# Optimization experiments

Measured on AMD Instinct MI355X. Metric: run time of the kernel, lower is better.

Reference implementation:

```python
import jax, jax.numpy as jnp
import numpy as np

N_PUZZLES = 512
N = N_PUZZLES * 81          # nodes
E = N_PUZZLES * 81 * 20     # edges (20 peers per cell)
H = 96                      # mlp_hidden == lstm_hidden
DE = 16                     # edge feature / embed dim


def _lin(key, din, dout):
    kw, kb = jax.random.split(key)
    s = 1.0 / np.sqrt(din)
    W = jax.random.uniform(kw, (din, dout), jnp.float32, -s, s)
    b = jax.random.uniform(kb, (dout,), jnp.float32, -s, s)
    return W, b


def setup_inputs() -> dict:
    key = jax.random.key(0)
    ks = jax.random.split(key, 16)
    inp = {}
    inp["puzzle"] = jax.random.normal(ks[0], (N, DE), jnp.float32)
    inp["nodes"] = jax.random.normal(ks[1], (N, H), jnp.float32)
    inp["edge_features"] = jax.random.normal(ks[2], (E, DE), jnp.float32)
    inp["h"] = jax.random.normal(ks[3], (N, H), jnp.float32)
    inp["c"] = jax.random.normal(ks[4], (N, H), jnp.float32)
    inp["edges"] = jax.random.randint(ks[5], (E, 2), 0, N, jnp.int64)
    # message MLP: in = 2*H + DE
    inp["msg_W1"], inp["msg_b1"] = _lin(ks[6], 2 * H + DE, H)
    inp["msg_W2"], inp["msg_b2"] = _lin(ks[7], H, H)
    inp["msg_W3"], inp["msg_b3"] = _lin(ks[8], H, H)
    # post MLP: in = H + DE
    inp["post_W1"], inp["post_b1"] = _lin(ks[9], H + DE, H)
    inp["post_W2"], inp["post_b2"] = _lin(ks[10], H, H)
    inp["post_W3"], inp["post_b3"] = _lin(ks[11], H, H)
    # LSTM step (torch gate order i,f,g,o)
    inp["W_ih"], inp["b_ih"] = _lin(ks[12], H, 4 * H)
    inp["W_hh"], inp["b_hh"] = _lin(ks[13], H, 4 * H)
    # output linear 96 -> 10
    inp["out_W"], inp["out_b"] = _lin(ks[14], H, 10)
    return inp


def _mlp3(x, W1, b1, W2, b2, W3, b3):
    x = x @ W1 + b1
    x = jax.nn.relu(x) @ W2 + b2
    x = jax.nn.relu(x) @ W3 + b3
    return x


def reference(puzzle, nodes, edge_features, h, c, edges,
              msg_W1, msg_b1, msg_W2, msg_b2, msg_W3, msg_b3,
              post_W1, post_b1, post_W2, post_b2, post_W3, post_b3,
              W_ih, b_ih, W_hh, b_hh, out_W, out_b):
    src = edges[:, 0]
    dst = edges[:, 1]
    # gather -> MLP -> scatter-sum (message passing)
    msg_in = jnp.concatenate([nodes[src], nodes[dst], edge_features], axis=1)  # [E, 2H+DE]
    m = _mlp3(msg_in, msg_W1, msg_b1, msg_W2, msg_b2, msg_W3, msg_b3)          # [E, H]
    agg = jax.ops.segment_sum(m, src, num_segments=nodes.shape[0])             # [N, H]
    # post MLP on [messages, puzzle embedding]
    x = _mlp3(jnp.concatenate([agg, puzzle], axis=1),
              post_W1, post_b1, post_W2, post_b2, post_W3, post_b3)            # [N, H]
    # single LSTM step (torch gate order: i, f, g, o)
    gates = x @ W_ih + b_ih + h @ W_hh + b_hh                                  # [N, 4H]
    i, f, g, o = jnp.split(gates, 4, axis=1)
    c_new = jax.nn.sigmoid(f) * c + jax.nn.sigmoid(i) * jnp.tanh(g)
    h_new = jax.nn.sigmoid(o) * jnp.tanh(c_new)
    out = (h_new @ out_W + out_b).reshape(-1, 81, 10)                          # [B, 81, 10]
    return (h_new, h_new, c_new, out)
```

## Files before the change

### kernel.cpp

```cpp
#include <hip/hip_runtime.h>

#define NN 41472
#define NE 829440

typedef __attribute__((ext_vector_type(8))) short short8;
typedef __attribute__((ext_vector_type(4))) float f32x4;
typedef __attribute__((ext_vector_type(16))) float f32x16;
typedef __attribute__((ext_vector_type(4))) float float4v;
typedef __attribute__((ext_vector_type(4))) unsigned u32x4;

#define FLG_OFF   0
#define AGG_OFF   256
#define AGG_BYTES 15925248
#define W1F_OFF   (AGG_OFF + AGG_BYTES)
#define W2F_OFF   (W1F_OFF + 39936)
#define W3F_OFF   (W2F_OFF + 18432)
#define P1F_OFF   (W3F_OFF + 18432)
#define P2F_OFF   (P1F_OFF + 24576)
#define P3F_OFF   (P2F_OFF + 18432)
#define IHF_OFF   (P3F_OFF + 18432)
#define HHF_OFF   (IHF_OFF + 73728)
#define NB16_OFF  (HHF_OFF + 73728)
#define CUR_OFF   (NB16_OFF + 7962624)
#define BSUM_OFF  (CUR_OFF + 165888)
#define SRT_OFF   (BSUM_OFF + 256)
#define SID_OFF   (SRT_OFF + 6635520)
#define EFB_OFF   (SID_OFF + 3317760)
#define WS_NEED   (EFB_OFF + 26542080)

static __device__ __forceinline__ float bf2f(short s) {
  unsigned u = ((unsigned)(unsigned short)s) << 16;
  return __builtin_bit_cast(float, u);
}
static __device__ __forceinline__ short f2bf(float f) {
  unsigned u = __builtin_bit_cast(unsigned, f);
  unsigned r = (u + 0x7fffu + ((u >> 16) & 1u)) >> 16;
  return (short)r;
}
static __device__ __forceinline__ unsigned cvtpk(float lo, float hi) {
  unsigned r;
  asm("v_cvt_pk_bf16_f32 %0, %1, %2" : "=v"(r) : "v"(lo), "v"(hi));
  return r;
}
static __device__ __forceinline__ f32x4 fzero() { f32x4 z = {0.f, 0.f, 0.f, 0.f}; return z; }
static __device__ __forceinline__ f32x16 f16zero() {
  f32x16 z;
#pragma unroll
  for (int i = 0; i < 16; ++i) z[i] = 0.f;
  return z;
}
static __device__ __forceinline__ short8 szero() { short8 z = {0,0,0,0,0,0,0,0}; return z; }
static __device__ __forceinline__ float sigm(float x) { return 1.f / (1.f + __expf(-x)); }
static __device__ __forceinline__ float tanh_f(float x) {
  float ax = fabsf(x);
  float e  = __expf(-2.f * ax);
  float t  = (1.f - e) / (1.f + e);
  return copysignf(t, x);
}
static __device__ __forceinline__ int clampn(int v) {
  unsigned u = (unsigned)v;
  return (u < (unsigned)NN) ? v : 0;
}
static __device__ __forceinline__ float ldf(const void* base, size_t i, int f32) {
  return f32 ? ((const float*)base)[i] : bf2f(((const short*)base)[i]);
}
static __device__ __forceinline__ short8 ld8(const void* base, size_t i, int f32) {
  if (f32) {
    const float* p = (const float*)base + i;
    float4v a = *(const float4v*)p;
    float4v b = *(const float4v*)(p + 4);
    u32x4 u;
    u[0] = cvtpk(a[0], a[1]); u[1] = cvtpk(a[2], a[3]);
    u[2] = cvtpk(b[0], b[1]); u[3] = cvtpk(b[2], b[3]);
    return __builtin_bit_cast(short8, u);
  }
  return *(const short8*)((const short*)base + i);
}
static __device__ __forceinline__ short8 ldrow8(const void* base, size_t i, int f32) {
  if (f32) {
    const float* p = (const float*)base + i;
    short8 r;
#pragma unroll
    for (int j = 0; j < 8; ++j) r[j] = f2bf(p[j]);
    return r;
  }
  return *(const short8*)((const short*)base + i);
}
static __device__ __forceinline__ int ldedge(const int* e, int flat, int e64) {
  return e64 ? e[2 * flat] : e[flat];
}

__global__ __launch_bounds__(64) void sniff_kernel(const unsigned* __restrict__ nodes_u,
                                                   const int* __restrict__ edges_i,
                                                   int* __restrict__ flags) {
  int l = threadIdx.x;
  int votes = 0;
  for (int i = l; i < 256; i += 64) {
    unsigned u = nodes_u[i];
    int ex = (int)((u >> 23) & 0xFFu);
    if (ex >= 116 && ex <= 134) votes++;
  }
  int z = 0;
  for (int i = l; i < 128; i += 64) if (edges_i[2 * i + 1] == 0) z++;
#pragma unroll
  for (int o = 32; o; o >>= 1) { votes += __shfl_down(votes, o); z += __shfl_down(z, o); }
  if (l == 0) {
    flags[0] = (votes >= 160) ? 1 : 0;
    flags[1] = (z == 128) ? 1 : 0;
  }
}

__global__ __launch_bounds__(256) void zero_all_kernel(float4v* __restrict__ agg4,
                                                       int* __restrict__ cur) {
  int i = blockIdx.x * 256 + threadIdx.x;
  agg4[i] = float4v{0.f, 0.f, 0.f, 0.f};
  if (i < NN) cur[i] = 0;
}

__global__ __launch_bounds__(256) void nb16hist_kernel(const void* __restrict__ nodes,
                                                       const char* __restrict__ ws,
                                                       short8* __restrict__ out,
                                                       const int* __restrict__ edges,
                                                       int* __restrict__ cnt) {
  const int f32 = ((const int*)(ws + FLG_OFF))[0];
  const int e64 = ((const int*)(ws + FLG_OFF))[1];
  int gid = blockIdx.x * 256 + threadIdx.x;
  int s = clampn(ldedge(edges, 2 * gid, e64));
  atomicAdd(&cnt[s], 1);
  if (gid < NN * 96 / 8) out[gid] = ld8(nodes, (size_t)gid * 8, f32);
}

__global__ __launch_bounds__(1024) void scan_local_kernel(int* __restrict__ cnt,
                                                          int* __restrict__ bsum) {
  __shared__ int tmp[1024];
  const int t = threadIdx.x;
  const int i = blockIdx.x * 1024 + t;
  int v = (i < NN) ? cnt[i] : 0;
  tmp[t] = v;
  __syncthreads();
  for (int ofs = 1; ofs < 1024; ofs <<= 1) {
    int x = (t >= ofs) ? tmp[t - ofs] : 0;
    __syncthreads();
    tmp[t] += x;
    __syncthreads();
  }
  if (i < NN) cnt[i] = tmp[t] - v;
  if (t == 1023) bsum[blockIdx.x] = tmp[1023];
}

__global__ __launch_bounds__(64) void scan_tops_kernel(int* __restrict__ bsum, int nb) {
  int l = threadIdx.x;
  int v = (l < nb) ? bsum[l] : 0;
  int x = v;
#pragma unroll
  for (int o = 1; o < 64; o <<= 1) {
    int y = __shfl_up(x, o);
    if (l >= o) x += y;
  }
  if (l < nb) bsum[l] = x - v;
}

__global__ __launch_bounds__(1024) void scan_add_kernel(int* __restrict__ cnt,
                                                        const int* __restrict__ bsum) {
  int i = blockIdx.x * 1024 + threadIdx.x;
  if (i < NN) cnt[i] += bsum[blockIdx.x];
}

__global__ __launch_bounds__(256) void scatter_kernel(const int* __restrict__ edges,
                                                      const void* __restrict__ ef,
                                                      const char* __restrict__ ws,
                                                      int* __restrict__ cur,
                                                      int2* __restrict__ sdst,
                                                      short* __restrict__ efb) {
  const int f32 = ((const int*)(ws + FLG_OFF))[0];
  const int e64 = ((const int*)(ws + FLG_OFF))[1];
  int e = blockIdx.x * 256 + threadIdx.x;
  int s = clampn(ldedge(edges, 2 * e, e64));
  int d = clampn(ldedge(edges, 2 * e + 1, e64));
  int pos = atomicAdd(&cur[s], 1);
  sdst[pos] = make_int2(s, d);
  short8 lo = ld8(ef, (size_t)e * 16, f32);
  short8 hi = ld8(ef, (size_t)e * 16 + 8, f32);
  *(short8*)(efb + (size_t)pos * 16) = lo;
  *(short8*)(efb + (size_t)pos * 16 + 8) = hi;
}

__global__ __launch_bounds__(64) void relayout_kernel(
    const void* __restrict__ mW1, const void* __restrict__ mW2, const void* __restrict__ mW3,
    const void* __restrict__ pW1, const void* __restrict__ pW2, const void* __restrict__ pW3,
    const void* __restrict__ Wih, const void* __restrict__ Whh, char* __restrict__ ws)
{
  const int f32 = ((const int*)(ws + FLG_OFF))[0];
  int c = blockIdx.x;
  int l = threadIdx.x;
  const void* W; int K, NOUT, NT, fmt32; size_t off;
  if (c < 39)       {          W = mW1; K = 208; NOUT = 96;  NT = 3;  off = W1F_OFF; fmt32 = 1; }
  else if (c < 57)  { c -= 39;  W = mW2; K = 96;  NOUT = 96;  NT = 3;  off = W2F_OFF; fmt32 = 1; }
  else if (c < 75)  { c -= 57;  W = mW3; K = 96;  NOUT = 96;  NT = 3;  off = W3F_OFF; fmt32 = 1; }
  else if (c < 99)  { c -= 75;  W = pW1; K = 112; NOUT = 96;  NT = 6;  off = P1F_OFF; fmt32 = 0; }
  else if (c < 117) { c -= 99;  W = pW2; K = 96;  NOUT = 96;  NT = 6;  off = P2F_OFF; fmt32 = 0; }
  else if (c < 135) { c -= 117; W = pW3; K = 96;  NOUT = 96;  NT = 6;  off = P3F_OFF; fmt32 = 0; }
  else if (c < 207) { c -= 135; W = Wih; K = 96;  NOUT = 384; NT = 24; off = IHF_OFF; fmt32 = 0; }
  else              { c -= 207; W = Whh; K = 96;  NOUT = 384; NT = 24; off = HHF_OFF; fmt32 = 0; }
  int ks = c / NT, nt = c % NT;
  short8 v;
#pragma unroll
  for (int j = 0; j < 8; ++j) {
    int k, n;
    if (fmt32) { k = ks * 16 + (l >> 5) * 8 + j; n = nt * 32 + (l & 31); }
    else       { k = ks * 32 + (l >> 4) * 8 + j; n = nt * 16 + (l & 15); }
    v[j] = (k < K) ? f2bf(ldf(W, (size_t)k * NOUT + n, f32)) : (short)0;
  }
  short8* dst = (short8*)(ws + off);
  dst[c * 64 + l] = v;
}

template<int SORTED>
__global__ __launch_bounds__(256, 2) void edge_kernel(
    const void* __restrict__ nodes, const void* __restrict__ ef,
    const int* __restrict__ edges,
    const void* __restrict__ b1, const void* __restrict__ b2, const void* __restrict__ b3,
    const char* __restrict__ ws, float* __restrict__ agg)
{
  __shared__ __align__(16) short w2f[9216];
  __shared__ __align__(16) short w3f[9216];
  __shared__ __align__(16) short act[4][3328];

  const int f32 = ((const int*)(ws + FLG_OFF))[0];
  const int e64 = ((const int*)(ws + FLG_OFF))[1];
  const short* nb16 = (const short*)(ws + NB16_OFF);
  const int2*  sdst = (const int2*)(ws + SRT_OFF);
  const short* efb  = (const short*)(ws + EFB_OFF);

  {
    const short8* s2 = (const short8*)(ws + W2F_OFF);
    const short8* s3 = (const short8*)(ws + W3F_OFF);
    short8* d2 = (short8*)w2f;
    short8* d3 = (short8*)w3f;
    for (int i = threadIdx.x; i < 1152; i += 256) d2[i] = s2[i];
    for (int i = threadIdx.x; i < 1152; i += 256) d3[i] = s3[i];
  }
  __syncthreads();

  const int wv  = threadIdx.x >> 6;
  const int l   = threadIdx.x & 63;
  const int e31 = l & 31;
  const int hi  = l >> 5;
  short* aw = act[wv];
  const short8* w1g = (const short8*)(ws + W1F_OFF);

  const float B1[3] = {ldf(b1, e31, f32), ldf(b1, 32 + e31, f32), ldf(b1, 64 + e31, f32)};
  const float B2[3] = {ldf(b2, e31, f32), ldf(b2, 32 + e31, f32), ldf(b2, 64 + e31, f32)};
  const float B3[3] = {ldf(b3, e31, f32), ldf(b3, 32 + e31, f32), ldf(b3, 64 + e31, f32)};

  const int nbat = NE / 128;
  const int chunk = (nbat + gridDim.x - 1) / gridDim.x;
  const int it0 = blockIdx.x * chunk;
  int it1 = it0 + chunk; if (it1 > nbat) it1 = nbat;

  for (int it = it0; it < it1; ++it) {
    const int base = it * 128 + wv * 32;
    const int eL = base + e31;
    int src, dst;
    if (SORTED) {
      int2 sd = sdst[eL];
      src = clampn(sd.x); dst = clampn(sd.y);
    } else {
      src = clampn(ldedge(edges, 2 * eL, e64));
      dst = clampn(ldedge(edges, 2 * eL + 1, e64));
    }

    f32x16 a0 = f16zero(), a1 = f16zero(), a2 = f16zero();

#pragma unroll
    for (int ks = 0; ks < 6; ++ks) {
      short8 a = SORTED ? *(const short8*)(nb16 + (size_t)src * 96 + ks * 16 + hi * 8)
                        : ld8(nodes, (size_t)src * 96 + ks * 16 + hi * 8, f32);
      a0 = __builtin_amdgcn_mfma_f32_32x32x16_bf16(a, w1g[(ks * 3 + 0) * 64 + l], a0, 0, 0, 0);
      a1 = __builtin_amdgcn_mfma_f32_32x32x16_bf16(a, w1g[(ks * 3 + 1) * 64 + l], a1, 0, 0, 0);
      a2 = __builtin_amdgcn_mfma_f32_32x32x16_bf16(a, w1g[(ks * 3 + 2) * 64 + l], a2, 0, 0, 0);
    }
#pragma unroll
    for (int ks = 6; ks < 12; ++ks) {
      short8 a = SORTED ? *(const short8*)(nb16 + (size_t)dst * 96 + (ks - 6) * 16 + hi * 8)
                        : ld8(nodes, (size_t)dst * 96 + (ks - 6) * 16 + hi * 8, f32);
      a0 = __builtin_amdgcn_mfma_f32_32x32x16_bf16(a, w1g[(ks * 3 + 0) * 64 + l], a0, 0, 0, 0);
      a1 = __builtin_amdgcn_mfma_f32_32x32x16_bf16(a, w1g[(ks * 3 + 1) * 64 + l], a1, 0, 0, 0);
      a2 = __builtin_amdgcn_mfma_f32_32x32x16_bf16(a, w1g[(ks * 3 + 2) * 64 + l], a2, 0, 0, 0);
    }
    {
      short8 a = SORTED ? *(const short8*)(efb + (size_t)eL * 16 + hi * 8)
                        : ld8(ef, (size_t)eL * 16 + hi * 8, f32);
      a0 = __builtin_amdgcn_mfma_f32_32x32x16_bf16(a, w1g[(12 * 3 + 0) * 64 + l], a0, 0, 0, 0);
      a1 = __builtin_amdgcn_mfma_f32_32x32x16_bf16(a, w1g[(12 * 3 + 1) * 64 + l], a1, 0, 0, 0);
      a2 = __builtin_amdgcn_mfma_f32_32x32x16_bf16(a, w1g[(12 * 3 + 2) * 64 + l], a2, 0, 0, 0);
    }
#pragma unroll
    for (int r = 0; r < 16; ++r) {
      int row = (r & 3) + 8 * (r >> 2) + 4 * hi;
      aw[row * 104 +  0 + e31] = f2bf(fmaxf(a0[r] + B1[0], 0.f));
      aw[row * 104 + 32 + e31] = f2bf(fmaxf(a1[r] + B1[1], 0.f));
      aw[row * 104 + 64 + e31] = f2bf(fmaxf(a2[r] + B1[2], 0.f));
    }
    asm volatile("s_waitcnt lgkmcnt(0)" ::: "memory");
    __builtin_amdgcn_sched_barrier(0);

    f32x16 c0 = f16zero(), c1 = f16zero(), c2 = f16zero();
#pragma unroll
    for (int ks = 0; ks < 6; ++ks) {
      short8 a = *(const short8*)&aw[e31 * 104 + ks * 16 + hi * 8];
      c0 = __builtin_amdgcn_mfma_f32_32x32x16_bf16(a, *(const short8*)&w2f[((ks * 3 + 0) * 64 + l) * 8], c0, 0, 0, 0);
      c1 = __builtin_amdgcn_mfma_f32_32x32x16_bf16(a, *(const short8*)&w2f[((ks * 3 + 1) * 64 + l) * 8], c1, 0, 0, 0);
      c2 = __builtin_amdgcn_mfma_f32_32x32x16_bf16(a, *(const short8*)&w2f[((ks * 3 + 2) * 64 + l) * 8], c2, 0, 0, 0);
    }
#pragma unroll
    for (int r = 0; r < 16; ++r) {
      int row = (r & 3) + 8 * (r >> 2) + 4 * hi;
      aw[row * 104 +  0 + e31] = f2bf(fmaxf(c0[r] + B2[0], 0.f));
      aw[row * 104 + 32 + e31] = f2bf(fmaxf(c1[r] + B2[1], 0.f));
      aw[row * 104 + 64 + e31] = f2bf(fmaxf(c2[r] + B2[2], 0.f));
    }
    asm volatile("s_waitcnt lgkmcnt(0)" ::: "memory");
    __builtin_amdgcn_sched_barrier(0);

    f32x16 d0 = f16zero(), d1 = f16zero(), d2 = f16zero();
#pragma unroll
    for (int ks = 0; ks < 6; ++ks) {
      short8 a = *(const short8*)&aw[e31 * 104 + ks * 16 + hi * 8];
      d0 = __builtin_amdgcn_mfma_f32_32x32x16_bf16(a, *(const short8*)&w3f[((ks * 3 + 0) * 64 + l) * 8], d0, 0, 0, 0);
      d1 = __builtin_amdgcn_mfma_f32_32x32x16_bf16(a, *(const short8*)&w3f[((ks * 3 + 1) * 64 + l) * 8], d1, 0, 0, 0);
      d2 = __builtin_amdgcn_mfma_f32_32x32x16_bf16(a, *(const short8*)&w3f[((ks * 3 + 2) * 64 + l) * 8], d2, 0, 0, 0);
    }
    asm volatile("s_waitcnt lgkmcnt(0)" ::: "memory");
    __builtin_amdgcn_sched_barrier(0);

    if (SORTED) {
      float s0 = 0.f, s1 = 0.f, s2 = 0.f;
      int cu = -1, cnt = 0;
#pragma unroll
      for (int g = 0; g < 8; ++g) {
#pragma unroll
        for (int j = 0; j < 4; ++j) {
          const int reg = (g >> 1) * 4 + j;
          float t0 = d0[reg], t1 = d1[reg], t2 = d2[reg];
          float p0 = __shfl(t0, l ^ 32, 64);
          float p1 = __shfl(t1, l ^ 32, 64);
          float p2 = __shfl(t2, l ^ 32, 64);
          float v0 = ((g & 1) == hi) ? t0 : p0;
          float v1 = ((g & 1) == hi) ? t1 : p1;
          float v2 = ((g & 1) == hi) ? t2 : p2;
          int nd = __shfl(src, 4 * g + j, 64);
          if (nd == cu) {
            s0 += v0; s1 += v1; s2 += v2; cnt++;
          } else {
            if (hi == 0 && cu >= 0) {
              atomicAdd(&agg[(size_t)cu * 96 +      e31], s0 + cnt * B3[0]);
              atomicAdd(&agg[(size_t)cu * 96 + 32 + e31], s1 + cnt * B3[1]);
              atomicAdd(&agg[(size_t)cu * 96 + 64 + e31], s2 + cnt * B3[2]);
            }
            cu = nd; s0 = v0; s1 = v1; s2 = v2; cnt = 1;
          }
        }
      }
      if (hi == 0 && cu >= 0) {
        atomicAdd(&agg[(size_t)cu * 96 +      e31], s0 + cnt * B3[0]);
        atomicAdd(&agg[(size_t)cu * 96 + 32 + e31], s1 + cnt * B3[1]);
        atomicAdd(&agg[(size_t)cu * 96 + 64 + e31], s2 + cnt * B3[2]);
      }
    } else {
#pragma unroll
      for (int r = 0; r < 16; ++r) {
        int row = (r & 3) + 8 * (r >> 2) + 4 * hi;
        int s = clampn(ldedge(edges, 2 * (base + row), e64));
        atomicAdd(&agg[(size_t)s * 96 +      e31], d0[r] + B3[0]);
        atomicAdd(&agg[(size_t)s * 96 + 32 + e31], d1[r] + B3[1]);
        atomicAdd(&agg[(size_t)s * 96 + 64 + e31], d2[r] + B3[2]);
      }
    }
  }
}

__global__ __launch_bounds__(512, 1) void node_kernel(
    const float* __restrict__ agg, const void* __restrict__ puzzle,
    const void* __restrict__ h, const void* __restrict__ c,
    const void* __restrict__ pb1, const void* __restrict__ pb2, const void* __restrict__ pb3,
    const void* __restrict__ bih, const void* __restrict__ bhh,
    const void* __restrict__ oW, const void* __restrict__ ob,
    const char* __restrict__ ws,
    float* __restrict__ oh0, float* __restrict__ oh1, float* __restrict__ oc,
    float* __restrict__ oo)
{
  __shared__ __align__(16) short p2f[9216];
  __shared__ __align__(16) short p3f[9216];
  __shared__ __align__(16) short act[8][16][104];

  const int f32 = ((const int*)(ws + FLG_OFF))[0];

  {
    const short8* s2 = (const short8*)(ws + P2F_OFF);
    const short8* s3 = (const short8*)(ws + P3F_OFF);
    short8* d2 = (short8*)p2f;
    short8* d3 = (short8*)p3f;
    for (int i = threadIdx.x; i < 1152; i += 512) d2[i] = s2[i];
    for (int i = threadIdx.x; i < 1152; i += 512) d3[i] = s3[i];
  }
  __syncthreads();

  const int wv = threadIdx.x >> 6;
  const int l  = threadIdx.x & 63;
  const int lg = l >> 4, lr = l & 15;
  const int n0 = blockIdx.x * 128 + wv * 16;
  const int row = n0 + lr;

  const short8* p1g = (const short8*)(ws + P1F_OFF);
  const short8* ihg = (const short8*)(ws + IHF_OFF);
  const short8* hhg = (const short8*)(ws + HHF_OFF);

  f32x4 acc[6];
#pragma unroll
  for (int nt = 0; nt < 6; ++nt) acc[nt] = fzero();

#pragma unroll
  for (int ks = 0; ks < 3; ++ks) {
    const float* p = agg + (size_t)row * 96 + ks * 32 + lg * 8;
    short8 ahi, alo;
#pragma unroll
    for (int j = 0; j < 8; ++j) {
      float v = p[j];
      short hiq = f2bf(v);
      ahi[j] = hiq;
      alo[j] = f2bf(v - bf2f(hiq));
    }
#pragma unroll
    for (int nt = 0; nt < 6; ++nt) {
      short8 b = p1g[(ks * 6 + nt) * 64 + l];
      acc[nt] = __builtin_amdgcn_mfma_f32_16x16x32_bf16(ahi, b, acc[nt], 0, 0, 0);
      acc[nt] = __builtin_amdgcn_mfma_f32_16x16x32_bf16(alo, b, acc[nt], 0, 0, 0);
    }
  }
  {
    short8 a;
    if (lg < 2) a = ldrow8(puzzle, (size_t)row * 16 + lg * 8, f32);
    else        a = szero();
#pragma unroll
    for (int nt = 0; nt < 6; ++nt) {
      short8 b = p1g[(3 * 6 + nt) * 64 + l];
      acc[nt] = __builtin_amdgcn_mfma_f32_16x16x32_bf16(a, b, acc[nt], 0, 0, 0);
    }
  }
#pragma unroll
  for (int nt = 0; nt < 6; ++nt) {
    float bb = ldf(pb1, nt * 16 + lr, f32);
#pragma unroll
    for (int r = 0; r < 4; ++r) {
      float v = fmaxf(acc[nt][r] + bb, 0.f);
      act[wv][lg * 4 + r][nt * 16 + lr] = f2bf(v);
    }
    acc[nt] = fzero();
  }
  __syncthreads();

#pragma unroll
  for (int ks = 0; ks < 3; ++ks) {
    short8 a = *(const short8*)&act[wv][lr][ks * 32 + lg * 8];
#pragma unroll
    for (int nt = 0; nt < 6; ++nt) {
      short8 b = *(const short8*)&p2f[((ks * 6 + nt) * 64 + l) * 8];
      acc[nt] = __builtin_amdgcn_mfma_f32_16x16x32_bf16(a, b, acc[nt], 0, 0, 0);
    }
  }
  __syncthreads();
#pragma unroll
  for (int nt = 0; nt < 6; ++nt) {
    float bb = ldf(pb2, nt * 16 + lr, f32);
#pragma unroll
    for (int r = 0; r < 4; ++r) {
      float v = fmaxf(acc[nt][r] + bb, 0.f);
      act[wv][lg * 4 + r][nt * 16 + lr] = f2bf(v);
    }
    acc[nt] = fzero();
  }
  __syncthreads();

#pragma unroll
  for (int ks = 0; ks < 3; ++ks) {
    short8 a = *(const short8*)&act[wv][lr][ks * 32 + lg * 8];
#pragma unroll
    for (int nt = 0; nt < 6; ++nt) {
      short8 b = *(const short8*)&p3f[((ks * 6 + nt) * 64 + l) * 8];
      acc[nt] = __builtin_amdgcn_mfma_f32_16x16x32_bf16(a, b, acc[nt], 0, 0, 0);
    }
  }
  __syncthreads();
#pragma unroll
  for (int nt = 0; nt < 6; ++nt) {
    float bb = ldf(pb3, nt * 16 + lr, f32);
#pragma unroll
    for (int r = 0; r < 4; ++r) {
      act[wv][lg * 4 + r][nt * 16 + lr] = f2bf(acc[nt][r] + bb);
    }
  }
  __syncthreads();

  f32x4 g[24];
#pragma unroll
  for (int nt = 0; nt < 24; ++nt) g[nt] = fzero();
#pragma unroll
  for (int ks = 0; ks < 3; ++ks) {
    short8 ax = *(const short8*)&act[wv][lr][ks * 32 + lg * 8];
    short8 ah = ldrow8(h, (size_t)row * 96 + ks * 32 + lg * 8, f32);
#pragma unroll
    for (int nt = 0; nt < 24; ++nt) {
      short8 bi = ihg[(ks * 24 + nt) * 64 + l];
      g[nt] = __builtin_amdgcn_mfma_f32_16x16x32_bf16(ax, bi, g[nt], 0, 0, 0);
      short8 bh = hhg[(ks * 24 + nt) * 64 + l];
      g[nt] = __builtin_amdgcn_mfma_f32_16x16x32_bf16(ah, bh, g[nt], 0, 0, 0);
    }
  }

#pragma unroll
  for (int nt = 0; nt < 6; ++nt) {
    int col = nt * 16 + lr;
    float bi_i = ldf(bih, col, f32)       + ldf(bhh, col, f32);
    float bi_f = ldf(bih, 96 + col, f32)  + ldf(bhh, 96 + col, f32);
    float bi_g = ldf(bih, 192 + col, f32) + ldf(bhh, 192 + col, f32);
    float bi_o = ldf(bih, 288 + col, f32) + ldf(bhh, 288 + col, f32);
#pragma unroll
    for (int r = 0; r < 4; ++r) {
      int node = n0 + lg * 4 + r;
      float iv = g[nt][r]      + bi_i;
      float fv = g[nt + 6][r]  + bi_f;
      float gv = g[nt + 12][r] + bi_g;
      float ov = g[nt + 18][r] + bi_o;
      float cv = ldf(c, (size_t)node * 96 + col, f32);
      float cn = sigm(fv) * cv + sigm(iv) * tanh_f(gv);
      float hn = sigm(ov) * tanh_f(cn);
      oh0[(size_t)node * 96 + col] = hn;
      oh1[(size_t)node * 96 + col] = hn;
      oc [(size_t)node * 96 + col] = cn;
      act[wv][lg * 4 + r][col] = f2bf(hn);
    }
  }
  __syncthreads();

  const int nb0 = blockIdx.x * 128;
  for (int idx = threadIdx.x; idx < 1280; idx += 512) {
    int node16 = idx / 10;
    int o = idx - node16 * 10;
    const short* hrow = &act[node16 >> 4][node16 & 15][0];
    float a2 = ldf(ob, o, f32);
    for (int k = 0; k < 96; ++k)
      a2 = fmaf(bf2f(hrow[k]), ldf(oW, (size_t)k * 10 + o, f32), a2);
    oo[(size_t)(nb0 + node16) * 10 + o] = a2;
  }
}

extern "C" void kernel_launch(void* const* d_in, const int* in_sizes, int n_in,
                              void* d_out, int out_size, void* d_ws, size_t ws_size,
                              hipStream_t stream)
{
  const void* puzzle = d_in[0];
  const void* nodes  = d_in[1];
  const void* ef     = d_in[2];
  const void* h      = d_in[3];
  const void* c      = d_in[4];
  const int*  edges  = (const int*)d_in[5];
  const void* mW1 = d_in[6];  const void* mb1 = d_in[7];
  const void* mW2 = d_in[8];  const void* mb2 = d_in[9];
  const void* mW3 = d_in[10]; const void* mb3 = d_in[11];
  const void* pW1 = d_in[12]; const void* pb1 = d_in[13];
  const void* pW2 = d_in[14]; const void* pb2 = d_in[15];
  const void* pW3 = d_in[16]; const void* pb3 = d_in[17];
  const void* Wih = d_in[18]; const void* bih = d_in[19];
  const void* Whh = d_in[20]; const void* bhh = d_in[21];
  const void* oW  = d_in[22]; const void* ob  = d_in[23];

  char*  ws  = (char*)d_ws;
  int* flags = (int*)(ws + FLG_OFF);
  float* agg = (float*)(ws + AGG_OFF);
  int* cur = (int*)(ws + CUR_OFF);
  float* out = (float*)d_out;
  float* oh0 = out;
  float* oh1 = out + (size_t)NN * 96;
  float* oc  = out + (size_t)2 * NN * 96;
  float* oo  = out + (size_t)3 * NN * 96;

  sniff_kernel<<<1, 64, 0, stream>>>((const unsigned*)nodes, edges, flags);
  zero_all_kernel<<<3888, 256, 0, stream>>>((float4v*)agg, cur);
  relayout_kernel<<<279, 64, 0, stream>>>(mW1, mW2, mW3, pW1, pW2, pW3, Wih, Whh, ws);

  if (ws_size >= (size_t)WS_NEED) {
    int* bsum = (int*)(ws + BSUM_OFF);
    int2* sdst = (int2*)(ws + SRT_OFF);
    short* efb = (short*)(ws + EFB_OFF);
    const int nb = (NN + 1023) / 1024;

    nb16hist_kernel<<<NE / 256, 256, 0, stream>>>(nodes, ws, (short8*)(ws + NB16_OFF),
                                                  edges, cur);
    scan_local_kernel<<<nb, 1024, 0, stream>>>(cur, bsum);
    scan_tops_kernel<<<1, 64, 0, stream>>>(bsum, nb);
    scan_add_kernel<<<nb, 1024, 0, stream>>>(cur, bsum);
    scatter_kernel<<<NE / 256, 256, 0, stream>>>(edges, ef, ws, cur, sdst, efb);
    edge_kernel<1><<<512, 256, 0, stream>>>(nodes, ef, edges, mb1, mb2, mb3, ws, agg);
  } else {
    edge_kernel<0><<<512, 256, 0, stream>>>(nodes, ef, edges, mb1, mb2, mb3, ws, agg);
  }

  node_kernel<<<NN / 128, 512, 0, stream>>>(agg, puzzle, h, c, pb1, pb2, pb3, bih, bhh,
                                            oW, ob, ws, oh0, oh1, oc, oo);
}
```

Before: 372.1 us.

## Shrink node kernel blocks and replace block barriers with per-wave syncs

The node kernel now runs 256-thread blocks of 64 nodes instead of 512-thread blocks of 128, with launch bounds allowing two blocks per CU. Each wave works only on its own LDS activation tile, so block-wide __syncthreads between MLP stages become per-wave LDS waits. The output linear is now computed per wave on its own 16 nodes. The aim is to remove block barrier stalls and raise occupancy. The cost is that the p2f/p3f weight copy into LDS is repeated across twice as many blocks.

Result: faster. 318.3 us (median of 2 runs) (-14.5%).

```diff
diff --git a/kernel.cpp b/kernel.cpp
--- a/kernel.cpp
+++ b/kernel.cpp
@@ -8,6 +8,9 @@
 typedef __attribute__((ext_vector_type(16))) float f32x16;
 typedef __attribute__((ext_vector_type(4))) float float4v;
 typedef __attribute__((ext_vector_type(4))) unsigned u32x4;
+
+#define WAVESYNC() do { asm volatile("s_waitcnt lgkmcnt(0)" ::: "memory"); \
+                        __builtin_amdgcn_sched_barrier(0); } while (0)
 
 #define FLG_OFF   0
 #define AGG_OFF   256
@@ -302,8 +305,7 @@
       aw[row * 104 + 32 + e31] = f2bf(fmaxf(a1[r] + B1[1], 0.f));
       aw[row * 104 + 64 + e31] = f2bf(fmaxf(a2[r] + B1[2], 0.f));
     }
-    asm volatile("s_waitcnt lgkmcnt(0)" ::: "memory");
-    __builtin_amdgcn_sched_barrier(0);
+    WAVESYNC();
 
     f32x16 c0 = f16zero(), c1 = f16zero(), c2 = f16zero();
 #pragma unroll
@@ -320,8 +322,7 @@
       aw[row * 104 + 32 + e31] = f2bf(fmaxf(c1[r] + B2[1], 0.f));
       aw[row * 104 + 64 + e31] = f2bf(fmaxf(c2[r] + B2[2], 0.f));
     }
-    asm volatile("s_waitcnt lgkmcnt(0)" ::: "memory");
-    __builtin_amdgcn_sched_barrier(0);
+    WAVESYNC();
 
     f32x16 d0 = f16zero(), d1 = f16zero(), d2 = f16zero();
 #pragma unroll
@@ -331,8 +332,7 @@
       d1 = __builtin_amdgcn_mfma_f32_32x32x16_bf16(a, *(const short8*)&w3f[((ks * 3 + 1) * 64 + l) * 8], d1, 0, 0, 0);
       d2 = __builtin_amdgcn_mfma_f32_32x32x16_bf16(a, *(const short8*)&w3f[((ks * 3 + 2) * 64 + l) * 8], d2, 0, 0, 0);
     }
-    asm volatile("s_waitcnt lgkmcnt(0)" ::: "memory");
-    __builtin_amdgcn_sched_barrier(0);
+    WAVESYNC();
 
     if (SORTED) {
       float s0 = 0.f, s1 = 0.f, s2 = 0.f;
@@ -380,7 +380,7 @@
   }
 }
 
-__global__ __launch_bounds__(512, 1) void node_kernel(
+__global__ __launch_bounds__(256, 2) void node_kernel(
     const float* __restrict__ agg, const void* __restrict__ puzzle,
     const void* __restrict__ h, const void* __restrict__ c,
     const void* __restrict__ pb1, const void* __restrict__ pb2, const void* __restrict__ pb3,
@@ -392,7 +392,7 @@
 {
   __shared__ __align__(16) short p2f[9216];
   __shared__ __align__(16) short p3f[9216];
-  __shared__ __align__(16) short act[8][16][104];
+  __shared__ __align__(16) short act[4][16][104];
 
   const int f32 = ((const int*)(ws + FLG_OFF))[0];
 
@@ -401,15 +401,15 @@
     const short8* s3 = (const short8*)(ws + P3F_OFF);
     short8* d2 = (short8*)p2f;
     short8* d3 = (short8*)p3f;
-    for (int i = threadIdx.x; i < 1152; i += 512) d2[i] = s2[i];
-    for (int i = threadIdx.x; i < 1152; i += 512) d3[i] = s3[i];
+    for (int i = threadIdx.x; i < 1152; i += 256) d2[i] = s2[i];
+    for (int i = threadIdx.x; i < 1152; i += 256) d3[i] = s3[i];
   }
   __syncthreads();
 
   const int wv = threadIdx.x >> 6;
   const int l  = threadIdx.x & 63;
   const int lg = l >> 4, lr = l & 15;
-  const int n0 = blockIdx.x * 128 + wv * 16;
+  const int n0 = blockIdx.x * 64 + wv * 16;
   const int row = n0 + lr;
 
   const short8* p1g = (const short8*)(ws + P1F_OFF);
@@ -458,7 +458,7 @@
     }
     acc[nt] = fzero();
   }
-  __syncthreads();
+  WAVESYNC();
 
 #pragma unroll
   for (int ks = 0; ks < 3; ++ks) {
@@ -469,7 +469,7 @@
       acc[nt] = __builtin_amdgcn_mfma_f32_16x16x32_bf16(a, b, acc[nt], 0, 0, 0);
     }
   }
-  __syncthreads();
+  WAVESYNC();
 #pragma unroll
   for (int nt = 0; nt < 6; ++nt) {
     float bb = ldf(pb2, nt * 16 + lr, f32);
@@ -480,7 +480,7 @@
     }
     acc[nt] = fzero();
   }
-  __syncthreads();
+  WAVESYNC();
 
 #pragma unroll
   for (int ks = 0; ks < 3; ++ks) {
@@ -491,7 +491,7 @@
       acc[nt] = __builtin_amdgcn_mfma_f32_16x16x32_bf16(a, b, acc[nt], 0, 0, 0);
     }
   }
-  __syncthreads();
+  WAVESYNC();
 #pragma unroll
   for (int nt = 0; nt < 6; ++nt) {
     float bb = ldf(pb3, nt * 16 + lr, f32);
@@ -500,7 +500,7 @@
       act[wv][lg * 4 + r][nt * 16 + lr] = f2bf(acc[nt][r] + bb);
     }
   }
-  __syncthreads();
+  WAVESYNC();
 
   f32x4 g[24];
 #pragma unroll
@@ -541,17 +541,16 @@
       act[wv][lg * 4 + r][col] = f2bf(hn);
     }
   }
-  __syncthreads();
-
-  const int nb0 = blockIdx.x * 128;
-  for (int idx = threadIdx.x; idx < 1280; idx += 512) {
-    int node16 = idx / 10;
-    int o = idx - node16 * 10;
-    const short* hrow = &act[node16 >> 4][node16 & 15][0];
+  WAVESYNC();
+
+  for (int idx = l; idx < 160; idx += 64) {
+    int nl = idx / 10;
+    int o = idx - nl * 10;
+    const short* hrow = &act[wv][nl][0];
     float a2 = ldf(ob, o, f32);
     for (int k = 0; k < 96; ++k)
       a2 = fmaf(bf2f(hrow[k]), ldf(oW, (size_t)k * 10 + o, f32), a2);
-    oo[(size_t)(nb0 + node16) * 10 + o] = a2;
+    oo[(size_t)(n0 + nl) * 10 + o] = a2;
   }
 }
 
@@ -606,6 +605,6 @@
     edge_kernel<0><<<512, 256, 0, stream>>>(nodes, ef, edges, mb1, mb2, mb3, ws, agg);
   }
 
-  node_kernel<<<NN / 128, 512, 0, stream>>>(agg, puzzle, h, c, pb1, pb2, pb3, bih, bhh,
-                                            oW, ob, ws, oh0, oh1, oc, oo);
-}
+  node_kernel<<<NN / 64, 256, 0, stream>>>(agg, puzzle, h, c, pb1, pb2, pb3, bih, bhh,
+                                           oW, ob, ws, oh0, oh1, oc, oo);
+}
```
